# Performance work log

Measured on AMD Instinct MI355X. Metric: run time of the kernel, lower is better.

The kernel has to match this reference:

```python
import jax, jax.numpy as jnp
import numpy as np

N_HEADS = 16
KEY_DIM = 64
VAL_DIM = 64
KV_CH = 512


def setup_inputs() -> dict:
    key = jax.random.key(0)
    k1, k2, k3, k4, k5, k6 = jax.random.split(key, 6)
    B, H, W = 32, 64, 64
    kv = jax.random.normal(k1, (B, H, W, KV_CH), dtype=jnp.float32)
    # 1x1 conv kernels are just [C_in, C_out] matrices
    scale = 1.0 / np.sqrt(KV_CH)
    W_k = jax.random.normal(k2, (KV_CH, N_HEADS * KEY_DIM), dtype=jnp.float32) * scale
    b_k = jnp.zeros((N_HEADS * KEY_DIM,), dtype=jnp.float32)
    W_v = jax.random.normal(k3, (KV_CH, N_HEADS * VAL_DIM), dtype=jnp.float32) * scale
    b_v = jnp.zeros((N_HEADS * VAL_DIM,), dtype=jnp.float32)
    query = jax.random.normal(k4, (1, 1, N_HEADS, KEY_DIM), dtype=jnp.float32) * 0.05
    return {"key_value": kv, "W_k": W_k, "b_k": b_k, "W_v": W_v, "b_v": b_v, "query": query}


def reference(key_value, W_k, b_k, W_v, b_v, query):
    B, H, W, _ = key_value.shape
    HW = H * W
    x = key_value.reshape(B, HW, KV_CH)  # 1x1 conv == per-pixel matmul
    key = (jnp.einsum('bsc,cd->bsd', x, W_k) + b_k).reshape(B, HW, N_HEADS, KEY_DIM)
    value = jnp.tanh(jnp.einsum('bsc,cd->bsd', x, W_v) + b_v).reshape(B, HW, N_HEADS, VAL_DIM)
    # query broadcast dot over key dim -> [B, HW, N]
    dot = jnp.einsum('bsnk,nk->bsn', key, query[0, 0])
    attn = jax.nn.softmax(dot, axis=1)  # softmax over spatial axis
    # inference mode: dropout is identity
    out = jnp.einsum('bsn,bsnv->bnv', attn, value)  # [B, N, V]
    return out
```

## Files before the change

### kernel.cpp

```cpp
#include <hip/hip_runtime.h>
#include <cstdint>

using short8 = __attribute__((ext_vector_type(8))) short;
using f32x4  = __attribute__((ext_vector_type(4))) float;

__device__ __forceinline__ unsigned short bf16rne(float f) {
  unsigned int u = __float_as_uint(f);
  unsigned int r = u + 0x7fffu + ((u >> 16) & 1u);
  return (unsigned short)(r >> 16);
}

__device__ __forceinline__ void gl2lds16(const void* g, void* s) {
  auto gp = reinterpret_cast<const __attribute__((address_space(1))) unsigned int*>(
      reinterpret_cast<uintptr_t>(g));
  auto sp = reinterpret_cast<__attribute__((address_space(3))) unsigned int*>(
      (uint32_t)reinterpret_cast<uintptr_t>(s));
  __builtin_amdgcn_global_load_lds(gp, sp, 16, 0, 0);
}

__device__ __forceinline__ float fast_tanh(float x) {
  float e = __expf(2.0f * x);
  return 1.0f - 2.0f / (e + 1.0f);
}

__global__ __launch_bounds__(256) void prep_kernel(
    const float* __restrict__ Wk, const float* __restrict__ q,
    const float* __restrict__ Wv,
    unsigned short* __restrict__ wqb, unsigned short* __restrict__ wvt) {
  __shared__ float T[64 * 65];
  int bid = blockIdx.x;
  if (bid < 32) {
    int idx = bid * 256 + threadIdx.x;
    int n = idx >> 9, c = idx & 511;
    const float* wrow = Wk + (long)c * 1024 + n * 64;
    const float* qrow = q + n * 64;
    float s = 0.f;
    #pragma unroll 8
    for (int k = 0; k < 64; ++k) s += wrow[k] * qrow[k];
    wqb[n * 512 + c] = bf16rne(s);
  } else {
    int t = bid - 32;
    int tc = t & 7, tl = t >> 3;
    int c0 = tc * 64, l0 = tl * 64;
    int j = threadIdx.x & 63, i0 = threadIdx.x >> 6;
    #pragma unroll
    for (int ii = 0; ii < 16; ++ii) {
      int i = i0 * 16 + ii;
      T[i * 65 + j] = Wv[(long)(c0 + i) * 1024 + l0 + j];
    }
    __syncthreads();
    #pragma unroll
    for (int ii = 0; ii < 16; ++ii) {
      int jj = i0 * 16 + ii;
      wvt[(long)(l0 + jj) * 512 + c0 + j] = bf16rne(T[j * 65 + jj]);
    }
  }
}

__global__ __launch_bounds__(256) void dot_kernel(
    const float* __restrict__ kv, const unsigned short* __restrict__ wqb,
    unsigned short* __restrict__ xb, float* __restrict__ dotbuf) {
  __shared__ __align__(16) unsigned short As[128 * 64];
  __shared__ __align__(16) unsigned short Ws[16 * 512];
  int tid = threadIdx.x;
  int l = tid & 63, w = tid >> 6;
  long row0 = (long)blockIdx.x * 128;

  for (int j = 0; j < 4; ++j) {
    int n = w * 4 + j;
    gl2lds16(wqb + n * 512 + ((l ^ (n & 7)) * 8), &Ws[n * 512]);
  }

  f32x4 acc[2];
  for (int mi = 0; mi < 2; ++mi) acc[mi] = f32x4{0.f, 0.f, 0.f, 0.f};

  for (int kb = 0; kb < 8; ++kb) {
    float4 fa[4][2];
    short8 ha[4];
    #pragma unroll
    for (int it = 0; it < 4; ++it) {
      int idx = it * 256 + tid;
      int r = idx >> 3, c8 = idx & 7;
      const float4* src = (const float4*)&kv[(row0 + r) * 512 + kb * 64 + c8 * 8];
      fa[it][0] = src[0];
      fa[it][1] = src[1];
      short8 h;
      h[0] = bf16rne(fa[it][0].x); h[1] = bf16rne(fa[it][0].y);
      h[2] = bf16rne(fa[it][0].z); h[3] = bf16rne(fa[it][0].w);
      h[4] = bf16rne(fa[it][1].x); h[5] = bf16rne(fa[it][1].y);
      h[6] = bf16rne(fa[it][1].z); h[7] = bf16rne(fa[it][1].w);
      ha[it] = h;
      *(short8*)&xb[(row0 + r) * 512 + kb * 64 + c8 * 8] = h;
    }
    __syncthreads();
    #pragma unroll
    for (int it = 0; it < 4; ++it) {
      int idx = it * 256 + tid;
      int r = idx >> 3, c8 = idx & 7;
      *(short8*)&As[r * 64 + ((c8 ^ (r & 7)) * 8)] = ha[it];
    }
    __syncthreads();
    #pragma unroll
    for (int k32 = 0; k32 < 2; ++k32) {
      int n = l & 15, qd = l >> 4;
      int cl = kb * 8 + k32 * 4 + qd;
      short8 bf = *(const short8*)&Ws[n * 512 + ((cl ^ (n & 7)) * 8)];
      int ch = k32 * 4 + qd;
      #pragma unroll
      for (int mi = 0; mi < 2; ++mi) {
        int m = w * 32 + mi * 16 + (l & 15);
        short8 af = *(const short8*)&As[m * 64 + ((ch ^ (l & 7)) * 8)];
        acc[mi] = __builtin_amdgcn_mfma_f32_16x16x32_bf16(af, bf, acc[mi], 0, 0, 0);
      }
    }
    __syncthreads();
  }
  int n = l & 15, qd = l >> 4;
  for (int mi = 0; mi < 2; ++mi) {
    long rg = row0 + w * 32 + mi * 16 + qd * 4;
    long b = rg >> 12;
    long s = rg & 4095;
    *(f32x4*)&dotbuf[((b * 16 + n) << 12) + s] = acc[mi];
  }
}

__global__ __launch_bounds__(256) void softmax_kernel(float* __restrict__ dotbuf) {
  long bn = blockIdx.x;
  float4* p = (float4*)(dotbuf + bn * 4096);
  int tid = threadIdx.x;
  int l = tid & 63, w = tid >> 6;
  float4 v[4];
  float mx = -1e30f;
  #pragma unroll
  for (int i = 0; i < 4; ++i) {
    v[i] = p[tid + i * 256];
    mx = fmaxf(mx, fmaxf(fmaxf(v[i].x, v[i].y), fmaxf(v[i].z, v[i].w)));
  }
  for (int o = 32; o; o >>= 1) mx = fmaxf(mx, __shfl_xor(mx, o, 64));
  __shared__ float redm[4];
  __shared__ float reds[4];
  if (l == 0) redm[w] = mx;
  __syncthreads();
  mx = fmaxf(fmaxf(redm[0], redm[1]), fmaxf(redm[2], redm[3]));
  float s = 0.f;
  #pragma unroll
  for (int i = 0; i < 4; ++i) {
    v[i].x = __expf(v[i].x - mx); v[i].y = __expf(v[i].y - mx);
    v[i].z = __expf(v[i].z - mx); v[i].w = __expf(v[i].w - mx);
    s += v[i].x + v[i].y + v[i].z + v[i].w;
  }
  for (int o = 32; o; o >>= 1) s += __shfl_xor(s, o, 64);
  if (l == 0) reds[w] = s;
  __syncthreads();
  s = reds[0] + reds[1] + reds[2] + reds[3];
  float inv = 1.0f / s;
  #pragma unroll
  for (int i = 0; i < 4; ++i) {
    v[i].x *= inv; v[i].y *= inv; v[i].z *= inv; v[i].w *= inv;
    p[tid + i * 256] = v[i];
  }
}

__global__ __launch_bounds__(256) void out_gemm_kernel(
    const unsigned short* __restrict__ xb, const unsigned short* __restrict__ wvt,
    const float* __restrict__ wn, const float* __restrict__ bv,
    float* __restrict__ out) {
  __shared__ __align__(16) unsigned short As[128 * 64];
  __shared__ __align__(16) unsigned short Bs[128 * 64];
  __shared__ float wlds[256];
  int tid = threadIdx.x;
  int l = tid & 63, w = tid >> 6;
  int wr = w >> 1, wc = w & 1;
  int lr = l >> 3, lc = l & 7;

  int id = blockIdx.x;
  int ct = (id >> 3) & 7;
  int g  = (id & 7) | ((id >> 6) << 3);
  int rt = g & 31;
  int b  = g >> 5;

  long row0 = ((long)b << 12) + rt * 128;
  long col0 = (long)ct * 128;
  const unsigned short* Ag = xb + row0 * 512;
  const unsigned short* Bg = wvt + col0 * 512;

  f32x4 acc[4][4];
  #pragma unroll
  for (int mi = 0; mi < 4; ++mi)
    #pragma unroll
    for (int ni = 0; ni < 4; ++ni) acc[mi][ni] = f32x4{0.f, 0.f, 0.f, 0.f};

  for (int kb = 0; kb < 8; ++kb) {
    __syncthreads();
    for (int j = 0; j < 4; ++j) {
      int jj = w * 4 + j;
      int r = jj * 8 + lr;
      int goff = r * 512 + kb * 64 + (lc ^ lr) * 8;
      gl2lds16(Ag + goff, &As[jj * 512]);
      gl2lds16(Bg + goff, &Bs[jj * 512]);
    }
    __syncthreads();
    #pragma unroll
    for (int k32 = 0; k32 < 2; ++k32) {
      int ch = k32 * 4 + (l >> 4);
      short8 af[4], bfr[4];
      #pragma unroll
      for (int mi = 0; mi < 4; ++mi) {
        int m = wr * 64 + mi * 16 + (l & 15);
        af[mi] = *(const short8*)&As[m * 64 + ((ch ^ (l & 7)) * 8)];
      }
      #pragma unroll
      for (int ni = 0; ni < 4; ++ni) {
        int n = wc * 64 + ni * 16 + (l & 15);
        bfr[ni] = *(const short8*)&Bs[n * 64 + ((ch ^ (l & 7)) * 8)];
      }
      #pragma unroll
      for (int mi = 0; mi < 4; ++mi)
        #pragma unroll
        for (int ni = 0; ni < 4; ++ni)
          acc[mi][ni] = __builtin_amdgcn_mfma_f32_16x16x32_bf16(af[mi], bfr[ni], acc[mi][ni], 0, 0, 0);
    }
  }

  int head0 = ct * 2;
  __syncthreads();
  {
    int hh = tid >> 7, r = tid & 127;
    wlds[tid] = wn[(((long)b * 16 + head0 + hh) << 12) + rt * 128 + r];
  }
  __syncthreads();
  int ngl = head0 + wc;
  int v0 = l & 15, qd = l >> 4;
  float bias[4];
  #pragma unroll
  for (int ni = 0; ni < 4; ++ni) bias[ni] = bv[ngl * 64 + ni * 16 + v0];
  float res[4] = {0.f, 0.f, 0.f, 0.f};
  #pragma unroll
  for (int mi = 0; mi < 4; ++mi) {
    int rb = wr * 64 + mi * 16 + qd * 4;
    float w0 = wlds[wc * 128 + rb + 0];
    float w1 = wlds[wc * 128 + rb + 1];
    float w2 = wlds[wc * 128 + rb + 2];
    float w3 = wlds[wc * 128 + rb + 3];
    #pragma unroll
    for (int ni = 0; ni < 4; ++ni) {
      f32x4 c = acc[mi][ni];
      res[ni] += w0 * fast_tanh(c[0] + bias[ni]) + w1 * fast_tanh(c[1] + bias[ni])
               + w2 * fast_tanh(c[2] + bias[ni]) + w3 * fast_tanh(c[3] + bias[ni]);
    }
  }
  #pragma unroll
  for (int ni = 0; ni < 4; ++ni) {
    float v = res[ni];
    v += __shfl_xor(v, 16, 64);
    v += __shfl_xor(v, 32, 64);
    if (qd == 0) atomicAdd(&out[b * 1024 + ngl * 64 + ni * 16 + v0], v);
  }
}

extern "C" void kernel_launch(void* const* d_in, const int* in_sizes, int n_in,
                              void* d_out, int out_size, void* d_ws, size_t ws_size,
                              hipStream_t stream) {
  const float* kv = (const float*)d_in[0];
  const float* Wk = (const float*)d_in[1];
  const float* Wv = (const float*)d_in[3];
  const float* bv = (const float*)d_in[4];
  const float* q  = (const float*)d_in[5];
  float* out = (float*)d_out;

  char* ws = (char*)d_ws;
  unsigned short* xb  = (unsigned short*)(ws);
  unsigned short* wqb = (unsigned short*)(ws + 134217728);
  unsigned short* wvt = (unsigned short*)(ws + 134217728 + 16384);
  float* dotbuf = (float*)(ws + 134217728 + 16384 + 1048576);

  hipMemsetAsync(d_out, 0, 32768 * sizeof(float), stream);
  prep_kernel<<<160, 256, 0, stream>>>(Wk, q, Wv, wqb, wvt);
  dot_kernel<<<1024, 256, 0, stream>>>(kv, wqb, xb, dotbuf);
  softmax_kernel<<<512, 256, 0, stream>>>(dotbuf);
  out_gemm_kernel<<<8192, 256, 0, stream>>>(xb, wvt, dotbuf, bv, out);
}
```

Before: 636.6 us.

## Double-buffer async DMA in dot and out GEMM kernels, enlarge output tile

The dot kernel now copies fp32 key_value tiles into LDS with async global-to-LDS loads, double-buffered, and converts them to bf16 from LDS inside the MFMA loop instead of staging through registers. The output GEMM moves to a 256x128 tile per block with K steps of 32, double-buffered DMA and one barrier per step. The grid is halved and occupancy is hinted at 2 blocks per SM. This aims to overlap global loads with MFMA work and raise data reuse, at the cost of more LDS and accumulator registers per block.

```diff
diff --git a/kernel.cpp b/kernel.cpp
--- a/kernel.cpp
+++ b/kernel.cpp
@@ -60,67 +60,61 @@
 __global__ __launch_bounds__(256) void dot_kernel(
     const float* __restrict__ kv, const unsigned short* __restrict__ wqb,
     unsigned short* __restrict__ xb, float* __restrict__ dotbuf) {
-  __shared__ __align__(16) unsigned short As[128 * 64];
+  __shared__ __align__(16) float AsF[2][128 * 64];
   __shared__ __align__(16) unsigned short Ws[16 * 512];
-  int tid = threadIdx.x;
-  int l = tid & 63, w = tid >> 6;
+  int tid = threadIdx.x, l = tid & 63, w = tid >> 6;
   long row0 = (long)blockIdx.x * 128;
+  int qd = l >> 4, lm = l & 15;
 
   for (int j = 0; j < 4; ++j) {
     int n = w * 4 + j;
     gl2lds16(wqb + n * 512 + ((l ^ (n & 7)) * 8), &Ws[n * 512]);
   }
 
+  auto dmaA = [&](int it, int buf) {
+    #pragma unroll
+    for (int j = 0; j < 8; ++j) {
+      int g = (w * 8 + j) * 64 + l;
+      int r = g >> 4, c = g & 15;
+      int cc = c ^ (r & 14);
+      gl2lds16(kv + (row0 + r) * 512 + it * 64 + cc * 4, &AsF[buf][(w * 8 + j) * 256]);
+    }
+  };
+
   f32x4 acc[2];
-  for (int mi = 0; mi < 2; ++mi) acc[mi] = f32x4{0.f, 0.f, 0.f, 0.f};
-
-  for (int kb = 0; kb < 8; ++kb) {
-    float4 fa[4][2];
-    short8 ha[4];
-    #pragma unroll
-    for (int it = 0; it < 4; ++it) {
-      int idx = it * 256 + tid;
-      int r = idx >> 3, c8 = idx & 7;
-      const float4* src = (const float4*)&kv[(row0 + r) * 512 + kb * 64 + c8 * 8];
-      fa[it][0] = src[0];
-      fa[it][1] = src[1];
-      short8 h;
-      h[0] = bf16rne(fa[it][0].x); h[1] = bf16rne(fa[it][0].y);
-      h[2] = bf16rne(fa[it][0].z); h[3] = bf16rne(fa[it][0].w);
-      h[4] = bf16rne(fa[it][1].x); h[5] = bf16rne(fa[it][1].y);
-      h[6] = bf16rne(fa[it][1].z); h[7] = bf16rne(fa[it][1].w);
-      ha[it] = h;
-      *(short8*)&xb[(row0 + r) * 512 + kb * 64 + c8 * 8] = h;
-    }
+  acc[0] = f32x4{0.f, 0.f, 0.f, 0.f};
+  acc[1] = f32x4{0.f, 0.f, 0.f, 0.f};
+
+  dmaA(0, 0);
+  for (int it = 0; it < 8; ++it) {
     __syncthreads();
-    #pragma unroll
-    for (int it = 0; it < 4; ++it) {
-      int idx = it * 256 + tid;
-      int r = idx >> 3, c8 = idx & 7;
-      *(short8*)&As[r * 64 + ((c8 ^ (r & 7)) * 8)] = ha[it];
-    }
-    __syncthreads();
-    #pragma unroll
-    for (int k32 = 0; k32 < 2; ++k32) {
-      int n = l & 15, qd = l >> 4;
-      int cl = kb * 8 + k32 * 4 + qd;
-      short8 bf = *(const short8*)&Ws[n * 512 + ((cl ^ (n & 7)) * 8)];
-      int ch = k32 * 4 + qd;
+    if (it < 7) dmaA(it + 1, (it + 1) & 1);
+    const float* base = &AsF[it & 1][0];
+    #pragma unroll
+    for (int mi = 0; mi < 2; ++mi) {
+      int m = w * 32 + mi * 16 + lm;
+      int s = m & 14;
       #pragma unroll
-      for (int mi = 0; mi < 2; ++mi) {
-        int m = w * 32 + mi * 16 + (l & 15);
-        short8 af = *(const short8*)&As[m * 64 + ((ch ^ (l & 7)) * 8)];
-        acc[mi] = __builtin_amdgcn_mfma_f32_16x16x32_bf16(af, bf, acc[mi], 0, 0, 0);
+      for (int k32 = 0; k32 < 2; ++k32) {
+        int fc = k32 * 8 + qd * 2;
+        float4 fa = *(const float4*)&base[(m * 16 + (fc ^ s)) * 4];
+        float4 fb = *(const float4*)&base[(m * 16 + ((fc + 1) ^ s)) * 4];
+        short8 h;
+        h[0] = bf16rne(fa.x); h[1] = bf16rne(fa.y); h[2] = bf16rne(fa.z); h[3] = bf16rne(fa.w);
+        h[4] = bf16rne(fb.x); h[5] = bf16rne(fb.y); h[6] = bf16rne(fb.z); h[7] = bf16rne(fb.w);
+        *(short8*)&xb[(row0 + m) * 512 + it * 64 + k32 * 32 + qd * 8] = h;
+        int cl = it * 8 + k32 * 4 + qd;
+        short8 bfrag = *(const short8*)&Ws[lm * 512 + ((cl ^ (lm & 7)) * 8)];
+        acc[mi] = __builtin_amdgcn_mfma_f32_16x16x32_bf16(h, bfrag, acc[mi], 0, 0, 0);
       }
     }
-    __syncthreads();
-  }
-  int n = l & 15, qd = l >> 4;
+  }
+  #pragma unroll
   for (int mi = 0; mi < 2; ++mi) {
     long rg = row0 + w * 32 + mi * 16 + qd * 4;
     long b = rg >> 12;
     long s = rg & 4095;
-    *(f32x4*)&dotbuf[((b * 16 + n) << 12) + s] = acc[mi];
+    *(f32x4*)&dotbuf[((b * 16 + lm) << 12) + s] = acc[mi];
   }
 }
 
@@ -161,100 +155,104 @@
   }
 }
 
-__global__ __launch_bounds__(256) void out_gemm_kernel(
+__global__ __launch_bounds__(256, 2) void out_gemm_kernel(
     const unsigned short* __restrict__ xb, const unsigned short* __restrict__ wvt,
     const float* __restrict__ wn, const float* __restrict__ bv,
     float* __restrict__ out) {
-  __shared__ __align__(16) unsigned short As[128 * 64];
-  __shared__ __align__(16) unsigned short Bs[128 * 64];
-  __shared__ float wlds[256];
-  int tid = threadIdx.x;
-  int l = tid & 63, w = tid >> 6;
-  int wr = w >> 1, wc = w & 1;
-  int lr = l >> 3, lc = l & 7;
+  __shared__ __align__(16) unsigned short As[2][8192];
+  __shared__ __align__(16) unsigned short Bs[2][4096];
+  __shared__ float wlds[512];
+  int tid = threadIdx.x, l = tid & 63, w = tid >> 6;
+  int qd = l >> 4, lm = l & 15;
 
   int id = blockIdx.x;
   int ct = (id >> 3) & 7;
-  int g  = (id & 7) | ((id >> 6) << 3);
-  int rt = g & 31;
-  int b  = g >> 5;
-
-  long row0 = ((long)b << 12) + rt * 128;
-  long col0 = (long)ct * 128;
+  int g = (id & 7) | ((id >> 6) << 3);
+  int rt = g & 15, b = g >> 4;
+  long row0 = ((long)b << 12) + rt * 256;
   const unsigned short* Ag = xb + row0 * 512;
-  const unsigned short* Bg = wvt + col0 * 512;
-
-  f32x4 acc[4][4];
+  const unsigned short* Bg = wvt + (long)ct * 128 * 512;
+
+  auto dma = [&](int it, int buf) {
+    #pragma unroll
+    for (int j = 0; j < 4; ++j) {
+      int pl = (w * 4 + j) * 64 + l;
+      int r2 = pl >> 3, sub = (pl & 7) ^ (r2 & 7);
+      int r = r2 * 2 + (sub >> 2), c = sub & 3;
+      gl2lds16(Ag + r * 512 + it * 32 + c * 8, &As[buf][(w * 4 + j) * 512]);
+    }
+    #pragma unroll
+    for (int j = 0; j < 2; ++j) {
+      int pl = (w * 2 + j) * 64 + l;
+      int r2 = pl >> 3, sub = (pl & 7) ^ (r2 & 7);
+      int r = r2 * 2 + (sub >> 2), c = sub & 3;
+      gl2lds16(Bg + r * 512 + it * 32 + c * 8, &Bs[buf][(w * 2 + j) * 512]);
+    }
+  };
+
+  f32x4 acc[4][8];
   #pragma unroll
   for (int mi = 0; mi < 4; ++mi)
     #pragma unroll
-    for (int ni = 0; ni < 4; ++ni) acc[mi][ni] = f32x4{0.f, 0.f, 0.f, 0.f};
-
-  for (int kb = 0; kb < 8; ++kb) {
+    for (int ni = 0; ni < 8; ++ni) acc[mi][ni] = f32x4{0.f, 0.f, 0.f, 0.f};
+
+  dma(0, 0);
+  for (int it = 0; it < 16; ++it) {
     __syncthreads();
-    for (int j = 0; j < 4; ++j) {
-      int jj = w * 4 + j;
-      int r = jj * 8 + lr;
-      int goff = r * 512 + kb * 64 + (lc ^ lr) * 8;
-      gl2lds16(Ag + goff, &As[jj * 512]);
-      gl2lds16(Bg + goff, &Bs[jj * 512]);
-    }
-    __syncthreads();
-    #pragma unroll
-    for (int k32 = 0; k32 < 2; ++k32) {
-      int ch = k32 * 4 + (l >> 4);
-      short8 af[4], bfr[4];
+    if (it < 15) dma(it + 1, (it + 1) & 1);
+    int buf = it & 1;
+    short8 bf[8];
+    #pragma unroll
+    for (int ni = 0; ni < 8; ++ni) {
+      int n = ni * 16 + lm;
+      int gi = (n >> 1) * 8 + (((((n & 1) << 2) | qd) ^ ((n >> 1) & 7)));
+      bf[ni] = *(const short8*)&Bs[buf][gi * 8];
+    }
+    #pragma unroll
+    for (int mi = 0; mi < 4; ++mi) {
+      int m = w * 64 + mi * 16 + lm;
+      int gi = (m >> 1) * 8 + (((((m & 1) << 2) | qd) ^ ((m >> 1) & 7)));
+      short8 af = *(const short8*)&As[buf][gi * 8];
       #pragma unroll
-      for (int mi = 0; mi < 4; ++mi) {
-        int m = wr * 64 + mi * 16 + (l & 15);
-        af[mi] = *(const short8*)&As[m * 64 + ((ch ^ (l & 7)) * 8)];
+      for (int ni = 0; ni < 8; ++ni)
+        acc[mi][ni] = __builtin_amdgcn_mfma_f32_16x16x32_bf16(af, bf[ni], acc[mi][ni], 0, 0, 0);
+    }
+  }
+
+  int head0 = ct * 2;
+  wlds[tid]       = wn[(((long)b * 16 + head0 + (tid >> 8)) << 12) + rt * 256 + (tid & 255)];
+  wlds[tid + 256] = wn[(((long)b * 16 + head0 + ((tid + 256) >> 8)) << 12) + rt * 256 + ((tid + 256) & 255)];
+  __syncthreads();
+
+  float bias[8];
+  #pragma unroll
+  for (int ni = 0; ni < 8; ++ni) bias[ni] = bv[(head0 + (ni >> 2)) * 64 + (ni & 3) * 16 + lm];
+  float res[8] = {0.f, 0.f, 0.f, 0.f, 0.f, 0.f, 0.f, 0.f};
+  #pragma unroll
+  for (int mi = 0; mi < 4; ++mi) {
+    int rb = w * 64 + mi * 16 + qd * 4;
+    #pragma unroll
+    for (int h = 0; h < 2; ++h) {
+      float w0 = wlds[h * 256 + rb + 0];
+      float w1 = wlds[h * 256 + rb + 1];
+      float w2 = wlds[h * 256 + rb + 2];
+      float w3 = wlds[h * 256 + rb + 3];
+      #pragma unroll
+      for (int nj = 0; nj < 4; ++nj) {
+        int ni = h * 4 + nj;
+        f32x4 c = acc[mi][ni];
+        res[ni] += w0 * fast_tanh(c[0] + bias[ni]) + w1 * fast_tanh(c[1] + bias[ni])
+                 + w2 * fast_tanh(c[2] + bias[ni]) + w3 * fast_tanh(c[3] + bias[ni]);
       }
-      #pragma unroll
-      for (int ni = 0; ni < 4; ++ni) {
-        int n = wc * 64 + ni * 16 + (l & 15);
-        bfr[ni] = *(const short8*)&Bs[n * 64 + ((ch ^ (l & 7)) * 8)];
-      }
-      #pragma unroll
-      for (int mi = 0; mi < 4; ++mi)
-        #pragma unroll
-        for (int ni = 0; ni < 4; ++ni)
-          acc[mi][ni] = __builtin_amdgcn_mfma_f32_16x16x32_bf16(af[mi], bfr[ni], acc[mi][ni], 0, 0, 0);
-    }
-  }
-
-  int head0 = ct * 2;
-  __syncthreads();
-  {
-    int hh = tid >> 7, r = tid & 127;
-    wlds[tid] = wn[(((long)b * 16 + head0 + hh) << 12) + rt * 128 + r];
-  }
-  __syncthreads();
-  int ngl = head0 + wc;
-  int v0 = l & 15, qd = l >> 4;
-  float bias[4];
-  #pragma unroll
-  for (int ni = 0; ni < 4; ++ni) bias[ni] = bv[ngl * 64 + ni * 16 + v0];
-  float res[4] = {0.f, 0.f, 0.f, 0.f};
-  #pragma unroll
-  for (int mi = 0; mi < 4; ++mi) {
-    int rb = wr * 64 + mi * 16 + qd * 4;
-    float w0 = wlds[wc * 128 + rb + 0];
-    float w1 = wlds[wc * 128 + rb + 1];
-    float w2 = wlds[wc * 128 + rb + 2];
-    float w3 = wlds[wc * 128 + rb + 3];
-    #pragma unroll
-    for (int ni = 0; ni < 4; ++ni) {
-      f32x4 c = acc[mi][ni];
-      res[ni] += w0 * fast_tanh(c[0] + bias[ni]) + w1 * fast_tanh(c[1] + bias[ni])
-               + w2 * fast_tanh(c[2] + bias[ni]) + w3 * fast_tanh(c[3] + bias[ni]);
-    }
-  }
-  #pragma unroll
-  for (int ni = 0; ni < 4; ++ni) {
+    }
+  }
+  #pragma unroll
+  for (int ni = 0; ni < 8; ++ni) {
     float v = res[ni];
     v += __shfl_xor(v, 16, 64);
     v += __shfl_xor(v, 32, 64);
-    if (qd == 0) atomicAdd(&out[b * 1024 + ngl * 64 + ni * 16 + v0], v);
+    if (qd == 0)
+      atomicAdd(&out[b * 1024 + (head0 + (ni >> 2)) * 64 + (ni & 3) * 16 + lm], v);
   }
 }
 
@@ -278,5 +276,5 @@
   prep_kernel<<<160, 256, 0, stream>>>(Wk, q, Wv, wqb, wvt);
   dot_kernel<<<1024, 256, 0, stream>>>(kv, wqb, xb, dotbuf);
   softmax_kernel<<<512, 256, 0, stream>>>(dotbuf);
-  out_gemm_kernel<<<8192, 256, 0, stream>>>(xb, wvt, dotbuf, bv, out);
-}
+  out_gemm_kernel<<<4096, 256, 0, stream>>>(xb, wvt, dotbuf, bv, out);
+}
```

Measured after the change: 578.6 us. 9.1% less time.
